# Kernel optimization log

Hardware: AMD Instinct MI355X
Metric: run time of the kernel (lower is better)

The kernel has to match this reference:

```python
import jax, jax.numpy as jnp
import numpy as np

B, N, F_IN = 8, 1024, 64
HEADS = 8
D = F_IN  # out_features per head (in_features == out_features)


def setup_inputs() -> dict:
    key = jax.random.key(0)
    ks = jax.random.split(key, 5)
    stdv = 1.0 / np.sqrt(F_IN * HEADS)
    h = jax.random.normal(ks[0], (B, N, F_IN), dtype=jnp.float32)
    adj = jnp.ones((B, N, N), dtype=jnp.float32)  # passed but unused by the module
    W = jax.random.uniform(ks[1], (F_IN, D * HEADS), minval=-stdv, maxval=stdv, dtype=jnp.float32)
    a = jax.random.uniform(ks[2], (2 * D, 1), minval=-stdv, maxval=stdv, dtype=jnp.float32)
    out_W = jax.random.normal(ks[3], (D * HEADS, F_IN), dtype=jnp.float32) / np.sqrt(D * HEADS)
    out_b = jnp.zeros((F_IN,), dtype=jnp.float32)
    return {"h": h, "adj": adj, "W": W, "a": a, "out_W": out_W, "out_b": out_b}


def reference(h, adj, W, a, out_W, out_b):
    Bv, Nv, _ = h.shape
    Dh = W.shape[1] // HEADS
    # Wh: [B, N, H, D]
    Wh = (h @ W).reshape(Bv, Nv, HEADS, Dh)
    # Additive attention decomposed: e[b,i,j,h] = leaky_relu(Wh[b,i,h].a_src + Wh[b,j,h].a_dst)
    a_src = jnp.einsum('bnhd,d->bnh', Wh, a[:Dh, 0])
    a_dst = jnp.einsum('bnhd,d->bnh', Wh, a[Dh:, 0])
    e = jax.nn.leaky_relu(a_src[:, :, None, :] + a_dst[:, None, :, :], negative_slope=0.01)  # [B,N,N,H]
    # Module applies softmax over dim=1 (the first node axis i)
    attn = jax.nn.softmax(e, axis=1)  # [B,N,N,H]
    # h_prime[b,i,h,:] = sum_j attn[b,i,j,h] * Wh[b,j,h,:]
    h_prime = jnp.einsum('bijh,bjhd->bihd', attn, Wh).reshape(Bv, Nv, HEADS * Dh)
    return h_prime @ out_W + out_b
```

## Files before the change

kernel.cpp:

```cpp
#include <hip/hip_runtime.h>


#define B_  8
#define N_  1024
#define H_  8
#define D_  64
#define BH_ 64
#define NCH 16
#define CLN 64

__global__ __launch_bounds__(256) void k_wh(
    const float* __restrict__ h, const float* __restrict__ W,
    const float* __restrict__ a,
    float* __restrict__ Wh, float* __restrict__ sArr, float* __restrict__ tArr) {
  __shared__ float hL[16 * 64];
  __shared__ float whL[16 * 512];
  __shared__ float aL[128];
  const int tid = threadIdx.x;
  const int row0 = blockIdx.x * 16;
  const int b = row0 >> 10;
  for (int i = tid; i < 16 * 64; i += 256) hL[i] = h[row0 * 64 + i];
  if (tid < 128) aL[tid] = a[tid];
  __syncthreads();

  float acc0[16], acc1[16];
#pragma unroll
  for (int r = 0; r < 16; ++r) { acc0[r] = 0.f; acc1[r] = 0.f; }
  for (int k = 0; k < 64; ++k) {
    const float w0 = W[k * 512 + tid];
    const float w1 = W[k * 512 + tid + 256];
#pragma unroll
    for (int r = 0; r < 16; ++r) {
      const float hv = hL[r * 64 + k];
      acc0[r] += hv * w0;
      acc1[r] += hv * w1;
    }
  }
  const int hh0 = tid >> 6, d0 = tid & 63;
  const int hh1 = (tid + 256) >> 6;
#pragma unroll
  for (int r = 0; r < 16; ++r) {
    const int n = (row0 + r) & (N_ - 1);
    whL[r * 512 + tid] = acc0[r];
    whL[r * 512 + tid + 256] = acc1[r];
    Wh[((b * H_ + hh0) * N_ + n) * D_ + d0] = acc0[r];
    Wh[((b * H_ + hh1) * N_ + n) * D_ + d0] = acc1[r];
  }
  __syncthreads();
  if (tid < 128) {
    const int r = tid >> 3, hh = tid & 7;
    const int n = (row0 + r) & (N_ - 1);
    float accS = 0.f, accT = 0.f;
    for (int jj = 0; jj < 64; ++jj) {
      const int d = (jj + tid) & 63;
      const float wv = whL[r * 512 + hh * 64 + d];
      accS += wv * aL[d];
      accT += wv * aL[64 + d];
    }
    sArr[(b * H_ + hh) * N_ + n] = accS;
    tArr[(b * H_ + hh) * N_ + n] = accT;
  }
}

__global__ __launch_bounds__(1024) void k_sort1(
    const float* __restrict__ sArr, const float* __restrict__ tArr,
    float* __restrict__ ssv, float* __restrict__ tsv, int* __restrict__ tsi) {
  __shared__ float vL[1024];
  __shared__ int   iL[1024];
  const int tid = threadIdx.x;
  const int bh = blockIdx.x >> 1;
  const bool isT = (blockIdx.x & 1) != 0;
  if (isT) {
    float v = tArr[bh * N_ + tid];
    int   idx = tid;
    for (int size = 2; size <= 1024; size <<= 1) {
      for (int stride = size >> 1; stride > 0; stride >>= 1) {
        const bool up = ((tid & size) == 0);
        const bool lower = ((tid & stride) == 0);
        float pv; int pi;
        if (stride >= 64) {
          __syncthreads();
          vL[tid] = v; iL[tid] = idx;
          __syncthreads();
          pv = vL[tid ^ stride]; pi = iL[tid ^ stride];
        } else {
          pv = __shfl_xor(v, stride);
          pi = __shfl_xor(idx, stride);
        }
        const bool sameDir = (up == lower);
        const bool pLess = (pv < v) || (pv == v && pi < idx);
        if (pLess == sameDir) { v = pv; idx = pi; }
      }
    }
    tsv[bh * N_ + tid] = v; tsi[bh * N_ + tid] = idx;
  } else {
    float v = sArr[bh * N_ + tid];
    for (int size = 2; size <= 1024; size <<= 1) {
      for (int stride = size >> 1; stride > 0; stride >>= 1) {
        const bool up = ((tid & size) == 0);
        const bool lower = ((tid & stride) == 0);
        float pv;
        if (stride >= 64) {
          __syncthreads();
          vL[tid] = v;
          __syncthreads();
          pv = vL[tid ^ stride];
        } else {
          pv = __shfl_xor(v, stride);
        }
        const bool sameDir = (up == lower);
        if ((pv < v) == sameDir) v = pv;
      }
    }
    ssv[bh * N_ + tid] = v;
  }
}

__global__ __launch_bounds__(1024) void k_mid2(
    const float* __restrict__ sArr,
    const float* __restrict__ ssv, const float* __restrict__ tsv,
    const int* __restrict__ tsi, const float* __restrict__ Wh,
    float* __restrict__ uArr, float* __restrict__ vArr,
    float* __restrict__ esG, float* __restrict__ es001G,
    int* __restrict__ startG, int* __restrict__ qListG,
    float* __restrict__ cOff1, float* __restrict__ cOff2,
    float* __restrict__ T1G) {
  __shared__ float sL[1024], tvL[1024];
  __shared__ int   tiL[1024];
  __shared__ float cum1L[1024], cum001L[1024];
  __shared__ float uL[1024], vL[1024];
  __shared__ int   cntL[1025], startL[1025];
  __shared__ float cs1[NCH * 64], cs2[NCH * 64];
  __shared__ float wf1[16], wf2[16];
  __shared__ int   wi1[16];
  const int tid = threadIdx.x, lane = tid & 63, wv = tid >> 6;
  const int bh = blockIdx.x;
  const int base = bh * N_;

  const float sv = ssv[base + tid];
  const float tj = tsv[base + tid];
  sL[tid] = sv; tvL[tid] = tj; tiL[tid] = tsi[base + tid];
  const float orig_s = sArr[base + tid];
  cntL[tid] = 0;
  if (tid == 0) cntL[1024] = 0;

  {
    float a1 = __expf(sv), a2 = __expf(0.01f * sv);
#pragma unroll
    for (int off = 1; off < 64; off <<= 1) {
      const float x1 = __shfl_up(a1, off);
      const float x2 = __shfl_up(a2, off);
      if (lane >= off) { a1 += x1; a2 += x2; }
    }
    if (lane == 63) { wf1[wv] = a1; wf2[wv] = a2; }
    __syncthreads();
    float o1 = 0.f, o2 = 0.f;
    for (int ww = 0; ww < 16; ++ww) {
      if (ww < wv) { o1 += wf1[ww]; o2 += wf2[ww]; }
    }
    cum1L[tid] = a1 + o1; cum001L[tid] = a2 + o2;
  }
  __syncthreads();
  const float totalHi = cum1L[1023];

  {
    const float th = -tj;
    int lo = 0, hi = 1024;
    while (lo < hi) { const int mid = (lo + hi) >> 1; if (sL[mid] <= th) lo = mid + 1; else hi = mid; }
    const float S_lo = (lo > 0) ? cum001L[lo - 1] : 0.f;
    const float S_hi = totalHi - ((lo > 0) ? cum1L[lo - 1] : 0.f);
    const float et = __expf(tj), et001 = __expf(0.01f * tj);
    const float Z = et * S_hi + et001 * S_lo;
    const float u = et / Z, v = et001 / Z;
    uL[tid] = u; vL[tid] = v;
    uArr[base + tid] = u; vArr[base + tid] = v;
  }

  int rk;
  {
    const float th = -orig_s;
    int lo = 0, hi = 1024;
    while (lo < hi) { const int mid = (lo + hi) >> 1; if (tvL[mid] <= th) lo = mid + 1; else hi = mid; }
    rk = lo;
    atomicAdd(&cntL[rk], 1);
    esG[base + tid] = __expf(orig_s);
    es001G[base + tid] = __expf(0.01f * orig_s);
  }
  __syncthreads();

  {
    const int cown = cntL[tid];
    int a = cown;
#pragma unroll
    for (int off = 1; off < 64; off <<= 1) {
      const int x = __shfl_up(a, off);
      if (lane >= off) a += x;
    }
    if (lane == 63) wi1[wv] = a;
    __syncthreads();
    int o = 0;
    for (int ww = 0; ww < 16; ++ww) {
      if (ww < wv) o += wi1[ww];
    }
    const int incl = a + o;
    startL[tid] = incl - cown;
    startG[bh * 1025 + tid] = incl - cown;
    if (tid == 1023) { startL[1024] = incl; startG[bh * 1025 + 1024] = incl; }
  }
  __syncthreads();
  cntL[tid] = 0;
  if (tid == 0) cntL[1024] = 0;
  __syncthreads();
  {
    const int pos = startL[rk] + atomicAdd(&cntL[rk], 1);
    qListG[base + pos] = tid;
  }

  {
    float s1 = 0.f, s2 = 0.f;
    for (int k2 = 0; k2 < CLN; ++k2) {
      const int k = wv * CLN + k2;
      const int j = tiL[k];
      const float w = Wh[(base + j) * D_ + lane];
      s1 += uL[k] * w;
      s2 += vL[k] * w;
    }
    cs1[wv * 64 + lane] = s1; cs2[wv * 64 + lane] = s2;
  }
  __syncthreads();

  {
    float o1 = 0.f, o2 = 0.f, T1 = 0.f;
    for (int m = 0; m < NCH; ++m) {
      const float v1 = cs1[m * 64 + lane];
      if (m < wv) { o1 += v1; o2 += cs2[m * 64 + lane]; }
      T1 += v1;
    }
    cOff1[(bh * NCH + wv) * 64 + lane] = o1;
    cOff2[(bh * NCH + wv) * 64 + lane] = o2;
    if (wv == NCH - 1) T1G[bh * 64 + lane] = T1;
  }
}

__global__ __launch_bounds__(64) void k_walk(
    const float* __restrict__ Wh, const int* __restrict__ tsi,
    const float* __restrict__ uArr, const float* __restrict__ vArr,
    const int* __restrict__ startG, const int* __restrict__ qListG,
    const float* __restrict__ esG, const float* __restrict__ es001G,
    const float* __restrict__ cOff1, const float* __restrict__ cOff2,
    const float* __restrict__ T1G, float* __restrict__ hp) {
  const int blk = blockIdx.x;
  const int bh = blk >> 4, c = blk & (NCH - 1);
  const int lane = threadIdx.x;
  const int b = bh >> 3, hh = bh & 7;
  const int base = bh * N_;

  float r1 = cOff1[blk * 64 + lane];
  float r2 = cOff2[blk * 64 + lane];
  const float T1 = T1G[bh * 64 + lane];
  const int   tiR = tsi[base + c * CLN + lane];
  const float uR  = uArr[base + c * CLN + lane];
  const float vR  = vArr[base + c * CLN + lane];
  const int   stR = startG[bh * 1025 + c * CLN + lane];
  const int   stEnd = startG[bh * 1025 + c * CLN + 64];

#pragma unroll 4
  for (int k2 = 0; k2 < CLN; ++k2) {
    const int qs = __shfl(stR, k2);
    const int qe = (k2 < 63) ? __shfl(stR, k2 + 1) : stEnd;
    for (int q = qs; q < qe; ++q) {
      const int i = qListG[base + q];
      const float es = esG[base + i], es001 = es001G[base + i];
      hp[((b * N_ + i) << 9) + (hh << 6) + lane] = es * (T1 - r1) + es001 * r2;
    }
    const int j = __shfl(tiR, k2);
    const float w = Wh[(base + j) * D_ + lane];
    r1 += __shfl(uR, k2) * w;
    r2 += __shfl(vR, k2) * w;
  }
  if (c == NCH - 1) {
    for (int q = stEnd; q < N_; ++q) {
      const int i = qListG[base + q];
      const float es = esG[base + i], es001 = es001G[base + i];
      hp[((b * N_ + i) << 9) + (hh << 6) + lane] = es * (T1 - r1) + es001 * r2;
    }
  }
}

__global__ __launch_bounds__(512) void k_out(
    const float* __restrict__ hp,
    const float* __restrict__ outW, const float* __restrict__ outb,
    float* __restrict__ out) {
  __shared__ float hpL[16 * 512];
  __shared__ float part[8 * 8 * 64];
  const int tid = threadIdx.x;
  const int row0 = blockIdx.x * 16;
  for (int i = tid; i < 16 * 512; i += 512) hpL[i] = hp[row0 * 512 + i];
  __syncthreads();

  const int cc = tid & 63, p = tid >> 6;
  float acc[16];
#pragma unroll
  for (int r = 0; r < 16; ++r) acc[r] = 0.f;
  for (int k = p * 64; k < p * 64 + 64; ++k) {
    const float wvv = outW[k * 64 + cc];
#pragma unroll
    for (int r = 0; r < 16; ++r) acc[r] += hpL[r * 512 + k] * wvv;
  }
  for (int half = 0; half < 2; ++half) {
#pragma unroll
    for (int r = 0; r < 8; ++r) part[(p * 8 + r) * 64 + cc] = acc[half * 8 + r];
    __syncthreads();
    {
      const int r = tid >> 6, c2 = tid & 63;
      float ssum = 0.f;
#pragma unroll
      for (int p2 = 0; p2 < 8; ++p2) ssum += part[(p2 * 8 + r) * 64 + c2];
      out[(row0 + half * 8 + r) * 64 + c2] = outb[c2] + ssum;
    }
    __syncthreads();
  }
}

extern "C" void kernel_launch(void* const* d_in, const int* in_sizes, int n_in,
                              void* d_out, int out_size, void* d_ws, size_t ws_size,
                              hipStream_t stream) {
  const float* h    = (const float*)d_in[0];
  const float* W    = (const float*)d_in[2];
  const float* a    = (const float*)d_in[3];
  const float* outW = (const float*)d_in[4];
  const float* outb = (const float*)d_in[5];
  float* out = (float*)d_out;

  float* ws    = (float*)d_ws;
  float* Wh    = ws;
  float* hpG   = Wh + (size_t)BH_ * N_ * D_;
  float* sArr  = hpG + (size_t)B_ * N_ * 512;
  float* tArr  = sArr + BH_ * N_;
  float* ssv   = tArr + BH_ * N_;
  float* tsv   = ssv + BH_ * N_;
  int*   tsi   = (int*)(tsv + BH_ * N_);
  float* uArr  = (float*)(tsi + BH_ * N_);
  float* vArr  = uArr + BH_ * N_;
  float* esG   = vArr + BH_ * N_;
  float* es001G= esG + BH_ * N_;
  int*   qListG= (int*)(es001G + BH_ * N_);
  int*   startG= qListG + BH_ * N_;
  float* cOff1 = (float*)(startG + BH_ * 1025);
  float* cOff2 = cOff1 + BH_ * NCH * 64;
  float* T1G   = cOff2 + BH_ * NCH * 64;

  hipLaunchKernelGGL(k_wh,    dim3((B_ * N_) / 16), dim3(256), 0, stream,
                     h, W, a, Wh, sArr, tArr);
  hipLaunchKernelGGL(k_sort1, dim3(BH_ * 2), dim3(1024), 0, stream,
                     sArr, tArr, ssv, tsv, tsi);
  hipLaunchKernelGGL(k_mid2,  dim3(BH_), dim3(1024), 0, stream,
                     sArr, ssv, tsv, tsi, Wh,
                     uArr, vArr, esG, es001G, startG, qListG, cOff1, cOff2, T1G);
  hipLaunchKernelGGL(k_walk,  dim3(BH_ * NCH), dim3(64), 0, stream,
                     Wh, tsi, uArr, vArr, startG, qListG, esG, es001G,
                     cOff1, cOff2, T1G, hpG);
  hipLaunchKernelGGL(k_out,   dim3((B_ * N_) / 16), dim3(512), 0, stream,
                     hpG, outW, outb, out);
}
```

Before: 190.8 us.

## Fuse mid and walk kernels into one block per head using shared memory

Merges the prefix-sum/bucketing kernel and the walk kernel into a single kernel, so each wave handles its own chunk. Wh values are kept in registers and the query list with its exp factors is packed into shared memory. This removes one launch and several global round-trips for u, v, es, start, qList and the chunk offsets. In exchange, only 64 blocks (one per batch-head) do the scattered hp writes, which limits parallelism. There is also heavy register pressure from the 64-element wreg array combined with the 1024-thread launch bound.

```diff
diff --git a/kernel.cpp b/kernel.cpp
--- a/kernel.cpp
+++ b/kernel.cpp
@@ -116,25 +116,23 @@
   }
 }
 
-__global__ __launch_bounds__(1024) void k_mid2(
+__global__ __launch_bounds__(1024, 4) void k_mid3(
     const float* __restrict__ sArr,
     const float* __restrict__ ssv, const float* __restrict__ tsv,
     const int* __restrict__ tsi, const float* __restrict__ Wh,
-    float* __restrict__ uArr, float* __restrict__ vArr,
-    float* __restrict__ esG, float* __restrict__ es001G,
-    int* __restrict__ startG, int* __restrict__ qListG,
-    float* __restrict__ cOff1, float* __restrict__ cOff2,
-    float* __restrict__ T1G) {
+    float* __restrict__ hp) {
   __shared__ float sL[1024], tvL[1024];
   __shared__ int   tiL[1024];
   __shared__ float cum1L[1024], cum001L[1024];
   __shared__ float uL[1024], vL[1024];
   __shared__ int   cntL[1025], startL[1025];
+  __shared__ float4 qPack[1024];
   __shared__ float cs1[NCH * 64], cs2[NCH * 64];
   __shared__ float wf1[16], wf2[16];
   __shared__ int   wi1[16];
   const int tid = threadIdx.x, lane = tid & 63, wv = tid >> 6;
   const int bh = blockIdx.x;
+  const int b = bh >> 3, hh = bh & 7;
   const int base = bh * N_;
 
   const float sv = ssv[base + tid];
@@ -171,9 +169,7 @@
     const float S_hi = totalHi - ((lo > 0) ? cum1L[lo - 1] : 0.f);
     const float et = __expf(tj), et001 = __expf(0.01f * tj);
     const float Z = et * S_hi + et001 * S_lo;
-    const float u = et / Z, v = et001 / Z;
-    uL[tid] = u; vL[tid] = v;
-    uArr[base + tid] = u; vArr[base + tid] = v;
+    uL[tid] = et / Z; vL[tid] = et001 / Z;
   }
 
   int rk;
@@ -183,8 +179,6 @@
     while (lo < hi) { const int mid = (lo + hi) >> 1; if (tvL[mid] <= th) lo = mid + 1; else hi = mid; }
     rk = lo;
     atomicAdd(&cntL[rk], 1);
-    esG[base + tid] = __expf(orig_s);
-    es001G[base + tid] = __expf(0.01f * orig_s);
   }
   __syncthreads();
 
@@ -204,8 +198,7 @@
     }
     const int incl = a + o;
     startL[tid] = incl - cown;
-    startG[bh * 1025 + tid] = incl - cown;
-    if (tid == 1023) { startL[1024] = incl; startG[bh * 1025 + 1024] = incl; }
+    if (tid == 1023) startL[1024] = incl;
   }
   __syncthreads();
   cntL[tid] = 0;
@@ -213,15 +206,19 @@
   __syncthreads();
   {
     const int pos = startL[rk] + atomicAdd(&cntL[rk], 1);
-    qListG[base + pos] = tid;
-  }
-
+    qPack[pos] = make_float4(__int_as_float(tid), __expf(orig_s),
+                             __expf(0.01f * orig_s), 0.f);
+  }
+
+  float wreg[CLN];
   {
     float s1 = 0.f, s2 = 0.f;
+#pragma unroll
     for (int k2 = 0; k2 < CLN; ++k2) {
       const int k = wv * CLN + k2;
       const int j = tiL[k];
       const float w = Wh[(base + j) * D_ + lane];
+      wreg[k2] = w;
       s1 += uL[k] * w;
       s2 += vL[k] * w;
     }
@@ -229,60 +226,34 @@
   }
   __syncthreads();
 
-  {
-    float o1 = 0.f, o2 = 0.f, T1 = 0.f;
-    for (int m = 0; m < NCH; ++m) {
-      const float v1 = cs1[m * 64 + lane];
-      if (m < wv) { o1 += v1; o2 += cs2[m * 64 + lane]; }
-      T1 += v1;
-    }
-    cOff1[(bh * NCH + wv) * 64 + lane] = o1;
-    cOff2[(bh * NCH + wv) * 64 + lane] = o2;
-    if (wv == NCH - 1) T1G[bh * 64 + lane] = T1;
-  }
-}
-
-__global__ __launch_bounds__(64) void k_walk(
-    const float* __restrict__ Wh, const int* __restrict__ tsi,
-    const float* __restrict__ uArr, const float* __restrict__ vArr,
-    const int* __restrict__ startG, const int* __restrict__ qListG,
-    const float* __restrict__ esG, const float* __restrict__ es001G,
-    const float* __restrict__ cOff1, const float* __restrict__ cOff2,
-    const float* __restrict__ T1G, float* __restrict__ hp) {
-  const int blk = blockIdx.x;
-  const int bh = blk >> 4, c = blk & (NCH - 1);
-  const int lane = threadIdx.x;
-  const int b = bh >> 3, hh = bh & 7;
-  const int base = bh * N_;
-
-  float r1 = cOff1[blk * 64 + lane];
-  float r2 = cOff2[blk * 64 + lane];
-  const float T1 = T1G[bh * 64 + lane];
-  const int   tiR = tsi[base + c * CLN + lane];
-  const float uR  = uArr[base + c * CLN + lane];
-  const float vR  = vArr[base + c * CLN + lane];
-  const int   stR = startG[bh * 1025 + c * CLN + lane];
-  const int   stEnd = startG[bh * 1025 + c * CLN + 64];
-
-#pragma unroll 4
+  float r1 = 0.f, r2 = 0.f, T1 = 0.f;
+  for (int m = 0; m < NCH; ++m) {
+    const float v1 = cs1[m * 64 + lane];
+    if (m < wv) { r1 += v1; r2 += cs2[m * 64 + lane]; }
+    T1 += v1;
+  }
+
+  const int sBase = wv * CLN;
+#pragma unroll
   for (int k2 = 0; k2 < CLN; ++k2) {
-    const int qs = __shfl(stR, k2);
-    const int qe = (k2 < 63) ? __shfl(stR, k2 + 1) : stEnd;
+    const int K = sBase + k2;
+    const int qs = startL[K], qe = startL[K + 1];
     for (int q = qs; q < qe; ++q) {
-      const int i = qListG[base + q];
-      const float es = esG[base + i], es001 = es001G[base + i];
-      hp[((b * N_ + i) << 9) + (hh << 6) + lane] = es * (T1 - r1) + es001 * r2;
-    }
-    const int j = __shfl(tiR, k2);
-    const float w = Wh[(base + j) * D_ + lane];
-    r1 += __shfl(uR, k2) * w;
-    r2 += __shfl(vR, k2) * w;
-  }
-  if (c == NCH - 1) {
-    for (int q = stEnd; q < N_; ++q) {
-      const int i = qListG[base + q];
-      const float es = esG[base + i], es001 = es001G[base + i];
-      hp[((b * N_ + i) << 9) + (hh << 6) + lane] = es * (T1 - r1) + es001 * r2;
+      const float4 qp = qPack[q];
+      const int i = __float_as_int(qp.x);
+      hp[((b * N_ + i) << 9) + (hh << 6) + lane] =
+          qp.y * (T1 - r1) + qp.z * r2;
+    }
+    r1 += uL[K] * wreg[k2];
+    r2 += vL[K] * wreg[k2];
+  }
+  if (wv == NCH - 1) {
+    const int qs = startL[1024];
+    for (int q = qs; q < N_; ++q) {
+      const float4 qp = qPack[q];
+      const int i = __float_as_int(qp.x);
+      hp[((b * N_ + i) << 9) + (hh << 6) + lane] =
+          qp.y * (T1 - r1) + qp.z * r2;
     }
   }
 }
@@ -340,26 +311,13 @@
   float* ssv   = tArr + BH_ * N_;
   float* tsv   = ssv + BH_ * N_;
   int*   tsi   = (int*)(tsv + BH_ * N_);
-  float* uArr  = (float*)(tsi + BH_ * N_);
-  float* vArr  = uArr + BH_ * N_;
-  float* esG   = vArr + BH_ * N_;
-  float* es001G= esG + BH_ * N_;
-  int*   qListG= (int*)(es001G + BH_ * N_);
-  int*   startG= qListG + BH_ * N_;
-  float* cOff1 = (float*)(startG + BH_ * 1025);
-  float* cOff2 = cOff1 + BH_ * NCH * 64;
-  float* T1G   = cOff2 + BH_ * NCH * 64;
 
   hipLaunchKernelGGL(k_wh,    dim3((B_ * N_) / 16), dim3(256), 0, stream,
                      h, W, a, Wh, sArr, tArr);
   hipLaunchKernelGGL(k_sort1, dim3(BH_ * 2), dim3(1024), 0, stream,
                      sArr, tArr, ssv, tsv, tsi);
-  hipLaunchKernelGGL(k_mid2,  dim3(BH_), dim3(1024), 0, stream,
-                     sArr, ssv, tsv, tsi, Wh,
-                     uArr, vArr, esG, es001G, startG, qListG, cOff1, cOff2, T1G);
-  hipLaunchKernelGGL(k_walk,  dim3(BH_ * NCH), dim3(64), 0, stream,
-                     Wh, tsi, uArr, vArr, startG, qListG, esG, es001G,
-                     cOff1, cOff2, T1G, hpG);
+  hipLaunchKernelGGL(k_mid3,  dim3(BH_), dim3(1024), 0, stream,
+                     sArr, ssv, tsv, tsi, Wh, hpG);
   hipLaunchKernelGGL(k_out,   dim3((B_ * N_) / 16), dim3(512), 0, stream,
                      hpG, outW, outb, out);
 }
```

New measurement: 159.2 us. 16.5% less time.

## Pack query records into float4 and split walk into prefix pass then scatter

Applied to the files above, without the earlier changes.

The mid kernel now writes each query's index, exp(s), exp(0.01 s) and its rank bucket as one float4 record instead of three separate arrays. It also takes u/v from registers via shuffles instead of shared memory. The walk kernel first computes the running prefix sums for all 64 positions of its chunk and stores them in shared memory, then runs one flat loop over the chunk's queries. Each query does a single float4 load and a shared-memory lookup. This removes the dependent index-then-gather loads and the data-dependent inner loop nested in the serial accumulation, at the cost of about 33KB of shared memory per 64-thread block, which may limit occupancy.

```diff
diff --git a/kernel.cpp b/kernel.cpp
--- a/kernel.cpp
+++ b/kernel.cpp
@@ -116,19 +116,17 @@
   }
 }
 
-__global__ __launch_bounds__(1024) void k_mid2(
+__global__ __launch_bounds__(1024) void k_mid4(
     const float* __restrict__ sArr,
     const float* __restrict__ ssv, const float* __restrict__ tsv,
     const int* __restrict__ tsi, const float* __restrict__ Wh,
     float* __restrict__ uArr, float* __restrict__ vArr,
-    float* __restrict__ esG, float* __restrict__ es001G,
-    int* __restrict__ startG, int* __restrict__ qListG,
+    float4* __restrict__ qPackG, int* __restrict__ startG,
     float* __restrict__ cOff1, float* __restrict__ cOff2,
     float* __restrict__ T1G) {
   __shared__ float sL[1024], tvL[1024];
   __shared__ int   tiL[1024];
   __shared__ float cum1L[1024], cum001L[1024];
-  __shared__ float uL[1024], vL[1024];
   __shared__ int   cntL[1025], startL[1025];
   __shared__ float cs1[NCH * 64], cs2[NCH * 64];
   __shared__ float wf1[16], wf2[16];
@@ -163,6 +161,7 @@
   __syncthreads();
   const float totalHi = cum1L[1023];
 
+  float uOwn, vOwn;
   {
     const float th = -tj;
     int lo = 0, hi = 1024;
@@ -171,9 +170,8 @@
     const float S_hi = totalHi - ((lo > 0) ? cum1L[lo - 1] : 0.f);
     const float et = __expf(tj), et001 = __expf(0.01f * tj);
     const float Z = et * S_hi + et001 * S_lo;
-    const float u = et / Z, v = et001 / Z;
-    uL[tid] = u; vL[tid] = v;
-    uArr[base + tid] = u; vArr[base + tid] = v;
+    uOwn = et / Z; vOwn = et001 / Z;
+    uArr[base + tid] = uOwn; vArr[base + tid] = vOwn;
   }
 
   int rk;
@@ -183,8 +181,6 @@
     while (lo < hi) { const int mid = (lo + hi) >> 1; if (tvL[mid] <= th) lo = mid + 1; else hi = mid; }
     rk = lo;
     atomicAdd(&cntL[rk], 1);
-    esG[base + tid] = __expf(orig_s);
-    es001G[base + tid] = __expf(0.01f * orig_s);
   }
   __syncthreads();
 
@@ -213,17 +209,18 @@
   __syncthreads();
   {
     const int pos = startL[rk] + atomicAdd(&cntL[rk], 1);
-    qListG[base + pos] = tid;
+    qPackG[base + pos] = make_float4(__int_as_float(tid), __expf(orig_s),
+                                     __expf(0.01f * orig_s), __int_as_float(rk));
   }
 
   {
     float s1 = 0.f, s2 = 0.f;
+#pragma unroll
     for (int k2 = 0; k2 < CLN; ++k2) {
-      const int k = wv * CLN + k2;
-      const int j = tiL[k];
+      const int j = tiL[wv * CLN + k2];
       const float w = Wh[(base + j) * D_ + lane];
-      s1 += uL[k] * w;
-      s2 += vL[k] * w;
+      s1 += __shfl(uOwn, k2) * w;
+      s2 += __shfl(vOwn, k2) * w;
     }
     cs1[wv * 64 + lane] = s1; cs2[wv * 64 + lane] = s2;
   }
@@ -242,13 +239,13 @@
   }
 }
 
-__global__ __launch_bounds__(64) void k_walk(
+__global__ __launch_bounds__(64) void k_walk2(
     const float* __restrict__ Wh, const int* __restrict__ tsi,
     const float* __restrict__ uArr, const float* __restrict__ vArr,
-    const int* __restrict__ startG, const int* __restrict__ qListG,
-    const float* __restrict__ esG, const float* __restrict__ es001G,
+    const int* __restrict__ startG, const float4* __restrict__ qPackG,
     const float* __restrict__ cOff1, const float* __restrict__ cOff2,
     const float* __restrict__ T1G, float* __restrict__ hp) {
+  __shared__ float pre1[(CLN + 1) * 64], pre2[(CLN + 1) * 64];
   const int blk = blockIdx.x;
   const int bh = blk >> 4, c = blk & (NCH - 1);
   const int lane = threadIdx.x;
@@ -261,29 +258,29 @@
   const int   tiR = tsi[base + c * CLN + lane];
   const float uR  = uArr[base + c * CLN + lane];
   const float vR  = vArr[base + c * CLN + lane];
-  const int   stR = startG[bh * 1025 + c * CLN + lane];
-  const int   stEnd = startG[bh * 1025 + c * CLN + 64];
-
-#pragma unroll 4
+  const int   qs0 = startG[bh * 1025 + c * CLN];
+  const int   qe0 = startG[bh * 1025 + c * CLN + 64];
+
+#pragma unroll
   for (int k2 = 0; k2 < CLN; ++k2) {
-    const int qs = __shfl(stR, k2);
-    const int qe = (k2 < 63) ? __shfl(stR, k2 + 1) : stEnd;
-    for (int q = qs; q < qe; ++q) {
-      const int i = qListG[base + q];
-      const float es = esG[base + i], es001 = es001G[base + i];
-      hp[((b * N_ + i) << 9) + (hh << 6) + lane] = es * (T1 - r1) + es001 * r2;
-    }
     const int j = __shfl(tiR, k2);
     const float w = Wh[(base + j) * D_ + lane];
+    pre1[k2 * 64 + lane] = r1;
+    pre2[k2 * 64 + lane] = r2;
     r1 += __shfl(uR, k2) * w;
     r2 += __shfl(vR, k2) * w;
   }
-  if (c == NCH - 1) {
-    for (int q = stEnd; q < N_; ++q) {
-      const int i = qListG[base + q];
-      const float es = esG[base + i], es001 = es001G[base + i];
-      hp[((b * N_ + i) << 9) + (hh << 6) + lane] = es * (T1 - r1) + es001 * r2;
-    }
+  pre1[CLN * 64 + lane] = r1;
+  pre2[CLN * 64 + lane] = r2;
+  __syncthreads();
+
+  const int qEnd = (c == NCH - 1) ? N_ : qe0;
+  for (int q = qs0; q < qEnd; ++q) {
+    const float4 qp = qPackG[base + q];
+    const int i  = __float_as_int(qp.x);
+    const int k2 = __float_as_int(qp.w) - c * CLN;
+    hp[((b * N_ + i) << 9) + (hh << 6) + lane] =
+        qp.y * (T1 - pre1[k2 * 64 + lane]) + qp.z * pre2[k2 * 64 + lane];
   }
 }
 
@@ -342,10 +339,8 @@
   int*   tsi   = (int*)(tsv + BH_ * N_);
   float* uArr  = (float*)(tsi + BH_ * N_);
   float* vArr  = uArr + BH_ * N_;
-  float* esG   = vArr + BH_ * N_;
-  float* es001G= esG + BH_ * N_;
-  int*   qListG= (int*)(es001G + BH_ * N_);
-  int*   startG= qListG + BH_ * N_;
+  float4* qPackG = (float4*)(vArr + BH_ * N_);
+  int*   startG  = (int*)(qPackG + BH_ * N_);
   float* cOff1 = (float*)(startG + BH_ * 1025);
   float* cOff2 = cOff1 + BH_ * NCH * 64;
   float* T1G   = cOff2 + BH_ * NCH * 64;
@@ -354,12 +349,11 @@
                      h, W, a, Wh, sArr, tArr);
   hipLaunchKernelGGL(k_sort1, dim3(BH_ * 2), dim3(1024), 0, stream,
                      sArr, tArr, ssv, tsv, tsi);
-  hipLaunchKernelGGL(k_mid2,  dim3(BH_), dim3(1024), 0, stream,
+  hipLaunchKernelGGL(k_mid4,  dim3(BH_), dim3(1024), 0, stream,
                      sArr, ssv, tsv, tsi, Wh,
-                     uArr, vArr, esG, es001G, startG, qListG, cOff1, cOff2, T1G);
-  hipLaunchKernelGGL(k_walk,  dim3(BH_ * NCH), dim3(64), 0, stream,
-                     Wh, tsi, uArr, vArr, startG, qListG, esG, es001G,
-                     cOff1, cOff2, T1G, hpG);
+                     uArr, vArr, qPackG, startG, cOff1, cOff2, T1G);
+  hipLaunchKernelGGL(k_walk2, dim3(BH_ * NCH), dim3(64), 0, stream,
+                     Wh, tsi, uArr, vArr, startG, qPackG, cOff1, cOff2, T1G, hpG);
   hipLaunchKernelGGL(k_out,   dim3((B_ * N_) / 16), dim3(512), 0, stream,
                      hpG, outW, outb, out);
 }
```

After: 163.1 us. -14.5%, faster.
